# Optimization experiments

Measured on AMD Instinct MI355X. Metric: run time of the kernel, lower is better.

Reference implementation:

```python
import jax, jax.numpy as jnp
from jax import lax
import numpy as np

B, S, D, H = 64, 256, 1024, 1024
NEG = -1e9


def setup_inputs() -> dict:
    key = jax.random.key(0)
    ks = jax.random.split(key, 8)
    sd = 1.0 / np.sqrt(D)
    sh = 1.0 / np.sqrt(H + 1)
    return {
        "lstm_features": jax.random.normal(ks[0], (B, S, D), jnp.float32),
        "mask": jnp.ones((B, S), jnp.int32),
        "Wl": jax.random.normal(ks[1], (D, H), jnp.float32) * sd,
        "bl": jnp.zeros((H,), jnp.float32),
        "Wr": jax.random.normal(ks[2], (D, H), jnp.float32) * sd,
        "br": jnp.zeros((H,), jnp.float32),
        "Wbil": jax.random.normal(ks[3], (H + 1, H + 1), jnp.float32) * sh,
        "bbil": jnp.zeros((), jnp.float32),
    }


def _span_scores(lstm_features, Wl, bl, Wr, br, Wbil, bbil):
    # left/right MLPs: Linear + LeakyReLU(0.1) (dropout=0 at inference)
    lefts = jax.nn.leaky_relu(lstm_features @ Wl + bl, 0.1)   # [B,S,H]
    rights = jax.nn.leaky_relu(lstm_features @ Wr + br, 0.1)  # [B,S,H]
    ones = jnp.ones(lefts.shape[:-1] + (1,), lefts.dtype)
    l1 = jnp.concatenate([lefts, ones], axis=-1)   # [B,S,H+1] (use_input_biases=True)
    r1 = jnp.concatenate([rights, ones], axis=-1)
    # bilinear: l1 @ W @ r1^T + bias  -> [B,S,S]
    return jnp.einsum('bsh,hg,btg->bst', l1, Wbil, r1) + bbil


def _cky(scores):
    """CKY over one [S,S] score matrix. chart[i,j]=scores[i,j]+max_s chart[i,s]+chart[s+1,j];
    singleton spans score 0. Returns (chart, best-split table)."""
    n = scores.shape[0]
    idx = jnp.arange(n)
    m = jnp.arange(n - 1)  # split offsets
    chart0 = jnp.zeros((n, n), scores.dtype)
    split0 = jnp.zeros((n, n), jnp.int32)

    def step(carry, w):
        chart, split = carry
        j = idx + w
        jc = jnp.clip(j, 0, n - 1)
        li = jnp.clip(idx[:, None] + m[None, :], 0, n - 1)       # left end
        ri = jnp.clip(idx[:, None] + m[None, :] + 1, 0, n - 1)   # right start
        cand = chart[idx[:, None], li] + chart[ri, jc[:, None]]  # [n, n-1]
        valid = (m[None, :] < w) & (j[:, None] < n)
        cand = jnp.where(valid, cand, NEG)
        val = scores[idx, jc] + jnp.max(cand, axis=1)
        bsplit = (idx + jnp.argmax(cand, axis=1)).astype(jnp.int32)
        ok = j < n
        chart = chart.at[idx, jc].set(jnp.where(ok, val, chart[idx, jc]))
        split = split.at[idx, jc].set(jnp.where(ok, bsplit, split[idx, jc]))
        return (chart, split), None

    (chart, split), _ = lax.scan(step, (chart0, split0), jnp.arange(1, n))
    return chart, split


def _backtrack(split):
    """Extract the n-1 internal spans of the best tree (fixed-size stack, jit-safe)."""
    n = split.shape[0]
    stack = jnp.full((2 * n, 2), -1, jnp.int32).at[0].set(jnp.array([0, n - 1], jnp.int32))
    out = jnp.zeros((n, 2), jnp.int32)

    def body(t, state):
        def do_pop(st):
            stack, top, out, cnt = st
            ij = stack[top - 1]
            i, j = ij[0], ij[1]
            top = top - 1
            out = out.at[cnt].set(ij)
            cnt = cnt + 1
            s = split[i, j]
            stack = stack.at[top].set(jnp.stack([i, s]))          # left child
            top = top + (s > i).astype(jnp.int32)
            stack = stack.at[top].set(jnp.stack([s + 1, j]))      # right child
            top = top + (j > s + 1).astype(jnp.int32)
            return (stack, top, out, cnt)
        return lax.cond(state[1] > 0, do_pop, lambda s: s, state)

    state = (stack, jnp.int32(1), out, jnp.int32(0))
    _, _, out, _ = lax.fori_loop(0, n - 1, body, state)
    return out  # [n,2] (lefts, rights), zero-padded like torch.zeros in original


def reference(lstm_features, mask, Wl, bl, Wr, br, Wbil, bbil):
    scores = _span_scores(lstm_features, Wl, bl, Wr, br, Wbil, bbil)  # [B,S,S]
    _, split = jax.vmap(_cky)(scores)
    spans = jax.vmap(_backtrack)(split)  # [B,S,2]
    ret_lefts = spans[..., 0].astype(jnp.int64)
    ret_rights = spans[..., 1].astype(jnp.int64)
    return ret_lefts, ret_rights
```

## Files before the change

kernel.cpp:

```cpp
#include <hip/hip_runtime.h>
#include <cstdint>


#define Bb 64
#define Ss 256
#define Dd 1024
#define Hh 1024

typedef __attribute__((ext_vector_type(8))) _Float16 f16x8;
typedef __attribute__((ext_vector_type(4))) float f32x4;

__device__ __forceinline__ void split2(float x, unsigned short& h,
                                       unsigned short& l) {
  _Float16 hh = (_Float16)x;
  _Float16 ll = (_Float16)(x - (float)hh);
  h = __builtin_bit_cast(unsigned short, hh);
  l = __builtin_bit_cast(unsigned short, ll);
}

__device__ __forceinline__ void gl_lds16(const void* g, void* l) {
  __builtin_amdgcn_global_load_lds(
      (const __attribute__((address_space(1))) void*)g,
      (__attribute__((address_space(3))) void*)l, 16, 0, 0);
}

__global__ __launch_bounds__(256) void splitw_kernel(
    const float* __restrict__ W, int ldw, unsigned short* __restrict__ O,
    long long plane) {
  int idx = blockIdx.x * 256 + threadIdx.x;
  int n = idx >> 10, k = idx & 1023;
  float x = W[(long long)k * ldw + n];
  unsigned short h, l;
  split2(x, h, l);
  O[idx] = h;
  O[plane + idx] = l;
}

__global__ __launch_bounds__(256) void bilvec_kernel(
    const float* __restrict__ Wbil, float* __restrict__ brow,
    float* __restrict__ bcol, float* __restrict__ corner) {
  int i = blockIdx.x * 256 + threadIdx.x;
  brow[i] = Wbil[1024 * 1025 + i];
  bcol[i] = Wbil[i * 1025 + 1024];
  if (i == 0) corner[0] = Wbil[1024 * 1025 + 1024];
}

__device__ __forceinline__ void pack8(char* dst, const unsigned short* v) {
  uint4 u;
  u.x = (unsigned)v[0] | ((unsigned)v[1] << 16);
  u.y = (unsigned)v[2] | ((unsigned)v[3] << 16);
  u.z = (unsigned)v[4] | ((unsigned)v[5] << 16);
  u.w = (unsigned)v[6] | ((unsigned)v[7] << 16);
  *(uint4*)dst = u;
}

__device__ __forceinline__ void split_store16f(const float* xs, char* lds,
                                               int base, int wa0, int wa1) {
  unsigned short hs[16], ls[16];
#pragma unroll
  for (int i = 0; i < 16; ++i) split2(xs[i], hs[i], ls[i]);
  pack8(&lds[base + wa0], hs);
  pack8(&lds[base + wa1], hs + 8);
  pack8(&lds[base + 8192 + wa0], ls);
  pack8(&lds[base + 8192 + wa1], ls + 8);
}

#define MFMA4(afv, bh, blv, accs, nf)                                        \
  {                                                                          \
    _Pragma("unroll") for (int mf = 0; mf < 4; ++mf) accs[mf][nf] =          \
        __builtin_amdgcn_mfma_f32_16x16x32_f16(afv[0][mf], bh,               \
                                               accs[mf][nf], 0, 0, 0);       \
    _Pragma("unroll") for (int mf = 0; mf < 4; ++mf) accs[mf][nf] =          \
        __builtin_amdgcn_mfma_f32_16x16x32_f16(afv[0][mf], blv,              \
                                               accs[mf][nf], 0, 0, 0);       \
    _Pragma("unroll") for (int mf = 0; mf < 4; ++mf) accs[mf][nf] =          \
        __builtin_amdgcn_mfma_f32_16x16x32_f16(afv[1][mf], bh,               \
                                               accs[mf][nf], 0, 0, 0);       \
    _Pragma("unroll") for (int mf = 0; mf < 4; ++mf) accs[mf][nf] =          \
        __builtin_amdgcn_mfma_f32_16x16x32_f16(afv[1][mf], blv,              \
                                               accs[mf][nf], 0, 0, 0);       \
  }

template <bool LEAKY>
__global__ __launch_bounds__(256, 3) void gemm_mfma_kernel(
    const float* __restrict__ A, const unsigned short* __restrict__ Bsp,
    long long bplane, float* __restrict__ C0, float* __restrict__ C1,
    const float* __restrict__ bias0, const float* __restrict__ bias1) {
  const int m0 = blockIdx.y * 128;
  const int n0 = blockIdx.x * 128;
  __shared__ __align__(16) char lds[49152];
  const int t = threadIdx.x;
  const int L = t & 63, w = t >> 6, q = L >> 4, l15 = L & 15;

  const int ar = t >> 1, ah = t & 1;
  const float* aptr = A + (long long)(m0 + ar) * 1024 + ah * 16;
  const int phiA = ((ar >> 1) ^ (ar >> 3)) & 3;
  const int wa0 = ar * 64 + (((2 * ah + 0) ^ phiA) << 4);
  const int wa1 = ar * 64 + (((2 * ah + 1) ^ phiA) << 4);

  int offA0[4], offB0[4];
#pragma unroll
  for (int f = 0; f < 4; ++f) {
    int rowa = ((w & 1) << 6) + (f << 4) + l15;
    offA0[f] = rowa * 64 + ((q ^ (((rowa >> 1) ^ (rowa >> 3)) & 3)) << 4);
    int rowb = ((w >> 1) << 6) + (f << 4) + l15;
    offB0[f] = rowb * 64 + ((q ^ (((rowb >> 1) ^ (rowb >> 3)) & 3)) << 4);
  }

  const int lrow = L >> 2, lchk = L & 3;
  const unsigned short* bsrc[4];
  int bldso[4];
#pragma unroll
  for (int i = 0; i < 4; ++i) {
    int O = ((w << 2) + i) << 10;
    int s2 = O >> 13;
    int r = ((O & 8191) >> 6) + lrow;
    int phi = ((r >> 1) ^ (r >> 3)) & 3;
    bsrc[i] = Bsp + (long long)s2 * bplane + (long long)(n0 + r) * 1024 +
              ((lchk ^ phi) << 3);
    bldso[i] = O;
  }

  f32x4 acc[4][4];
#pragma unroll
  for (int i = 0; i < 4; ++i)
#pragma unroll
    for (int j = 0; j < 4; ++j) acc[i][j] = (f32x4){0.f, 0.f, 0.f, 0.f};

#pragma unroll
  for (int i = 0; i < 4; ++i) gl_lds16(bsrc[i], &lds[16384 + bldso[i]]);
  float4 a0 = *(const float4*)(aptr + 0);
  float4 a1 = *(const float4*)(aptr + 4);
  float4 a2 = *(const float4*)(aptr + 8);
  float4 a3 = *(const float4*)(aptr + 12);

  int cur = 0;
  for (int k0 = 0; k0 < 1024; k0 += 32) {
    {
      float xs[16] = {a0.x, a0.y, a0.z, a0.w, a1.x, a1.y, a1.z, a1.w,
                      a2.x, a2.y, a2.z, a2.w, a3.x, a3.y, a3.z, a3.w};
      split_store16f(xs, lds, 0, wa0, wa1);
    }
    asm volatile("s_waitcnt vmcnt(0) lgkmcnt(0)\n\ts_barrier" ::: "memory");
    if (k0 < 992) {
      a0 = *(const float4*)(aptr + k0 + 32);
      a1 = *(const float4*)(aptr + k0 + 36);
      a2 = *(const float4*)(aptr + k0 + 40);
      a3 = *(const float4*)(aptr + k0 + 44);
      const int bn = 16384 + ((cur ^ 1) << 14);
#pragma unroll
      for (int i = 0; i < 4; ++i)
        gl_lds16(bsrc[i] + k0 + 32, &lds[bn + bldso[i]]);
    }
    const int bb = 16384 + (cur << 14);
    f16x8 af[2][4];
#pragma unroll
    for (int s = 0; s < 2; ++s)
#pragma unroll
      for (int f = 0; f < 4; ++f)
        af[s][f] = *(const f16x8*)&lds[s * 8192 + offA0[f]];
#pragma unroll
    for (int nf = 0; nf < 4; ++nf) {
      f16x8 bh = *(const f16x8*)&lds[bb + offB0[nf]];
      f16x8 bl = *(const f16x8*)&lds[bb + 8192 + offB0[nf]];
      MFMA4(af, bh, bl, acc, nf);
    }
    asm volatile("s_waitcnt lgkmcnt(0)\n\ts_barrier" ::: "memory");
    cur ^= 1;
  }

  const bool isR = (n0 >= 1024);
  float* Co = isR ? C1 : C0;
  const float* bp = isR ? bias1 : bias0;
  const int nc0 = n0 & 1023;
#pragma unroll
  for (int nf = 0; nf < 4; ++nf) {
    int col = nc0 + ((w >> 1) << 6) + (nf << 4) + l15;
    float bz = bp[col];
#pragma unroll
    for (int mf = 0; mf < 4; ++mf) {
#pragma unroll
      for (int r = 0; r < 4; ++r) {
        int row = m0 + ((w & 1) << 6) + (mf << 4) + (q << 2) + r;
        float x = acc[mf][nf][r] + bz;
        if (LEAKY) x = (x > 0.f) ? x : 0.1f * x;
        Co[(long long)row * 1024 + col] = x;
      }
    }
  }
}

__global__ __launch_bounds__(256, 3) void gemmnt_mfma_kernel(
    const float* __restrict__ A, const float* __restrict__ B,
    float* __restrict__ C, const float* __restrict__ rowAdd,
    const float* __restrict__ scal) {
  const int bz = blockIdx.z;
  A += (long long)bz * 256 * 1024;
  B += (long long)bz * 256 * 1024;
  C += (long long)bz * 256 * 256;
  const int m0 = blockIdx.y * 128;
  const int n0 = blockIdx.x * 128;
  __shared__ __align__(16) char lds[32768];
  const int t = threadIdx.x;
  const int L = t & 63, w = t >> 6, q = L >> 4, l15 = L & 15;

  const int ar = t >> 1, ah = t & 1;
  const float* aptr = A + (long long)(m0 + ar) * 1024 + ah * 16;
  const float* bptr = B + (long long)(n0 + ar) * 1024 + ah * 16;
  const int phiA = ((ar >> 1) ^ (ar >> 3)) & 3;
  const int wa0 = ar * 64 + (((2 * ah + 0) ^ phiA) << 4);
  const int wa1 = ar * 64 + (((2 * ah + 1) ^ phiA) << 4);

  int offA0[4], offB0[4];
#pragma unroll
  for (int f = 0; f < 4; ++f) {
    int rowa = ((w & 1) << 6) + (f << 4) + l15;
    offA0[f] = rowa * 64 + ((q ^ (((rowa >> 1) ^ (rowa >> 3)) & 3)) << 4);
    int rowb = ((w >> 1) << 6) + (f << 4) + l15;
    offB0[f] =
        16384 + rowb * 64 + ((q ^ (((rowb >> 1) ^ (rowb >> 3)) & 3)) << 4);
  }

  f32x4 acc[4][4];
#pragma unroll
  for (int i = 0; i < 4; ++i)
#pragma unroll
    for (int j = 0; j < 4; ++j) acc[i][j] = (f32x4){0.f, 0.f, 0.f, 0.f};

  float4 a0 = *(const float4*)(aptr + 0);
  float4 a1 = *(const float4*)(aptr + 4);
  float4 a2 = *(const float4*)(aptr + 8);
  float4 a3 = *(const float4*)(aptr + 12);
  float4 b0 = *(const float4*)(bptr + 0);
  float4 b1 = *(const float4*)(bptr + 4);
  float4 b2 = *(const float4*)(bptr + 8);
  float4 b3 = *(const float4*)(bptr + 12);

  for (int k0 = 0; k0 < 1024; k0 += 32) {
    {
      float xs[16] = {a0.x, a0.y, a0.z, a0.w, a1.x, a1.y, a1.z, a1.w,
                      a2.x, a2.y, a2.z, a2.w, a3.x, a3.y, a3.z, a3.w};
      split_store16f(xs, lds, 0, wa0, wa1);
      float ys[16] = {b0.x, b0.y, b0.z, b0.w, b1.x, b1.y, b1.z, b1.w,
                      b2.x, b2.y, b2.z, b2.w, b3.x, b3.y, b3.z, b3.w};
      split_store16f(ys, lds, 16384, wa0, wa1);
    }
    asm volatile("s_waitcnt lgkmcnt(0)\n\ts_barrier" ::: "memory");
    if (k0 < 992) {
      a0 = *(const float4*)(aptr + k0 + 32);
      a1 = *(const float4*)(aptr + k0 + 36);
      a2 = *(const float4*)(aptr + k0 + 40);
      a3 = *(const float4*)(aptr + k0 + 44);
      b0 = *(const float4*)(bptr + k0 + 32);
      b1 = *(const float4*)(bptr + k0 + 36);
      b2 = *(const float4*)(bptr + k0 + 40);
      b3 = *(const float4*)(bptr + k0 + 44);
    }
    f16x8 af[2][4];
#pragma unroll
    for (int s = 0; s < 2; ++s)
#pragma unroll
      for (int f = 0; f < 4; ++f)
        af[s][f] = *(const f16x8*)&lds[s * 8192 + offA0[f]];
#pragma unroll
    for (int nf = 0; nf < 4; ++nf) {
      f16x8 bh = *(const f16x8*)&lds[offB0[nf]];
      f16x8 bl = *(const f16x8*)&lds[8192 + offB0[nf]];
      MFMA4(af, bh, bl, acc, nf);
    }
    asm volatile("s_waitcnt lgkmcnt(0)\n\ts_barrier" ::: "memory");
  }

  const float sc_add = scal[0];
#pragma unroll
  for (int mf = 0; mf < 4; ++mf) {
#pragma unroll
    for (int r = 0; r < 4; ++r) {
      int row = m0 + ((w & 1) << 6) + (mf << 4) + (q << 2) + r;
      float radd = sc_add + rowAdd[(long long)bz * 256 + row];
#pragma unroll
      for (int nf = 0; nf < 4; ++nf) {
        int col = n0 + ((w >> 1) << 6) + (nf << 4) + l15;
        C[(long long)row * 256 + col] = acc[mf][nf][r] + radd;
      }
    }
  }
}

__global__ __launch_bounds__(64) void colvec_kernel(
    const float* __restrict__ lefts, const float* __restrict__ bcol,
    const float* __restrict__ corner, float* __restrict__ tmpb) {
  int row = blockIdx.x;
  int lane = threadIdx.x;
  const float* a = lefts + (long long)row * Hh;
  float s = 0.f;
#pragma unroll
  for (int h = lane; h < Hh; h += 64) s = fmaf(a[h], bcol[h], s);
#pragma unroll
  for (int off = 32; off > 0; off >>= 1) s += __shfl_down(s, off, 64);
  if (lane == 0) tmpb[row] = s + corner[0];
}

__global__ __launch_bounds__(1024) void cky_kernel(
    const float* __restrict__ scores,
    uint8_t* __restrict__ Sws,
    int* __restrict__ out)
{
  const int b = blockIdx.x;
  const int t = threadIdx.x;
  const int n = Ss;
  const float* sc = scores + (long long)b * n * n;
  uint8_t* SP = Sws + (long long)b * 32896;

  __shared__ float Dch[32896];
  __shared__ float pv[2][2048];
  __shared__ uint8_t pmv[2][2048];
  __shared__ int stk[256];

  const int offT[10] = {0,    256,  511,  765,  1018,
                        1270, 1521, 1771, 2020, 2268};

  if (t < n) {
    out[b * n + t] = 0;
    out[Bb * n + b * n + t] = 0;
    Dch[t] = 0.f;
  }

  float PS[10];
  PS[0] = 0.f;
#pragma unroll
  for (int w = 1; w <= 9; ++w) {
    int ic = t;
    if (ic > 255 - w) ic = 255 - w;
    PS[w] = sc[ic * 257 + w];
  }
  asm volatile("s_waitcnt lgkmcnt(0)\n\ts_barrier" ::: "memory");

#pragma unroll
  for (int w = 1; w <= 9; ++w) {
    const int nv = n - w;
    if (t < nv) {
      float bb = Dch[offT[w - 1] + t + 1];
      int bm = 0;
#pragma unroll
      for (int m = 1; m < 9; ++m) {
        if (m >= w) break;
        float c = Dch[offT[m] + t] + Dch[offT[w - 1 - m] + t + m + 1];
        if (c > bb) { bb = c; bm = m; }
      }
      const int off = w * 256 - ((w * (w - 1)) >> 1);
      Dch[off + t] = PS[w] + bb;
      SP[off + t] = (uint8_t)bm;
    }
    asm volatile("s_waitcnt lgkmcnt(0)\n\ts_barrier" ::: "memory");
  }

  auto run_b = [&](int W0b, int pbuf) {
    const int cnv = n - W0b - 4;
    int jb, gb, u, delta, lgGHL, SLOTG;
    if (cnv > 128) {
      const int p = t >> 7;
      jb = 3 - (p >> 1);
      gb = 1 - (p & 1);
      u = t & 127;
      delta = 128;
      lgGHL = 1;
      SLOTG = 256;
    } else {
      const int wid = t >> 6;
      jb = 3 - (wid >> 2);
      gb = 3 - (wid & 3);
      u = t & 63;
      delta = (cnv > 64) ? 64 : 0;
      lgGHL = 2;
      SLOTG = 128;
    }
    const int Wb = W0b + 4 + jb;
    const int nvb = n - Wb;
    int cnt = W0b - jb - 4;
    if (cnt < 0) cnt = 0;
    const int per = (cnt + (1 << lgGHL) - 1) >> lgGHL;
    const int mlo = jb + 4;
    int ml = mlo + gb * per;
    int mh = mlo + cnt;
    {
      int e = ml + per;
      if (e < mh) mh = e;
    }
    float b0 = -3.0e38f, b1 = -3.0e38f;
    int m0i = ml, m1i = ml;
    if (u < nvb && ml < mh) {
      int al = ml * n - ((ml * (ml - 1)) >> 1) + u;
      const int kr = Wb - 1 - ml;
      int ar = kr * n - ((kr * (kr - 1)) >> 1) + u + ml + 1;
      int dl = n - ml;
      int dr = n - Wb + ml + 1;
      if (delta) {
#pragma unroll 2
        for (int m = ml; m < mh; ++m) {
          float l0 = Dch[al], l1 = Dch[al + delta];
          float r0 = Dch[ar], r1 = Dch[ar + delta];
          float c0 = l0 + r0, c1 = l1 + r1;
          if (c0 > b0) { b0 = c0; m0i = m; }
          if (c1 > b1) { b1 = c1; m1i = m; }
          al += dl;
          ar -= dr;
          --dl;
          ++dr;
        }
      } else {
#pragma unroll 4
        for (int m = ml; m < mh; ++m) {
          float c = Dch[al] + Dch[ar];
          if (c > b0) { b0 = c; m0i = m; }
          al += dl;
          ar -= dr;
          --dl;
          ++dr;
        }
      }
    }
    const int slot = jb * 512 + gb * SLOTG + u;
    pv[pbuf][slot] = b0;
    pmv[pbuf][slot] = (uint8_t)m0i;
    if (delta) {
      pv[pbuf][slot + delta] = b1;
      pmv[pbuf][slot + delta] = (uint8_t)m1i;
    }
  };

  run_b(6, 0);
  asm volatile("s_waitcnt lgkmcnt(0)\n\ts_barrier" ::: "memory");

  const int wv = t >> 6, lane = t & 63;
  const int tcell = 61 * wv + lane;

  float scA[4];
#pragma unroll
  for (int j = 0; j < 4; ++j) {
    const int Wn = 10 + j;
    int ic = tcell;
    if (ic > 255 - Wn) ic = 255 - Wn;
    if (ic < 0) ic = 0;
    scA[j] = sc[ic * 257 + Wn];
  }

  for (int s = 3; s <= 64; ++s) {
    const int W0 = 4 * s - 2;
    const int nv1 = n - W0;
    const int pb = s & 1, po = pb ^ 1;
    const int nb = (nv1 + 60) / 61;

    float P4[4] = {0.f, 0.f, 0.f, 0.f};
    if (s < 64 && wv < nb) {
#pragma unroll
      for (int j = 0; j < 4; ++j) {
        const int Wn = W0 + 4 + j;
        int ic = tcell;
        if (ic > 255 - Wn) ic = 255 - Wn;
        if (ic < 0) ic = 0;
        P4[j] = sc[ic * 257 + Wn];
      }
    }

    if (wv < nb) {
      const int tc = (tcell < nv1) ? tcell : (nv1 - 1);
      const float* pvo = pv[po];
      const uint8_t* pmo = pmv[po];
      int GHa, SGa;
      if (nv1 > 128) { GHa = 2; SGa = 256; } else { GHa = 4; SGa = 128; }
      int offPB[4], offCB[4];
#pragma unroll
      for (int d = 0; d < 4; ++d) {
        const int dg = W0 - 4 + d;
        offPB[d] = dg * 256 - ((dg * (dg - 1)) >> 1);
        const int cg = W0 + d;
        offCB[d] = cg * 256 - ((cg * (cg - 1)) >> 1);
      }
      float VAL0, VAL1, VAL2, VAL3;
      float SH01, SH02, SH03, SH11, SH12, SH21;
      {
        const int W = W0;
        float bb = Dch[offPB[3] + tc + 1];
        int bm = 0;
#pragma unroll
        for (int dm = 1; dm < 4; ++dm) {
          const int m = dm;
          float c = Dch[offT[m] + tc] + Dch[offPB[3 - dm] + tc + m + 1];
          if (c > bb) { bb = c; bm = m; }
        }
#pragma unroll
        for (int g = 0; g < 4; ++g) {
          if (g >= GHa) break;
          const int sl = g * SGa + tc;
          float x = pvo[sl];
          if (x > bb) { bb = x; bm = pmo[sl]; }
        }
#pragma unroll
        for (int dr = 3; dr >= 0; --dr) {
          const int r = dr;
          const int m = W - 1 - r;
          float right = (r == 0) ? 0.f : Dch[offT[r] + tc + W - r];
          float c = Dch[offPB[3 - dr] + tc] + right;
          if (c > bb) { bb = c; bm = m; }
        }
        VAL0 = scA[0] + bb;
        if (tcell < nv1) {
          Dch[offCB[0] + tcell] = VAL0;
          SP[offCB[0] + tcell] = (uint8_t)bm;
        }
        SH01 = __shfl_down(VAL0, 1, 64);
        SH02 = __shfl_down(VAL0, 2, 64);
        SH03 = __shfl_down(VAL0, 3, 64);
      }
      {
        const int W = W0 + 1;
        float bb = SH01;
        int bm = 0;
#pragma unroll
        for (int dm = 0; dm < 4; ++dm) {
          const int m = 1 + dm;
          float c = Dch[offT[m] + tc] + Dch[offPB[3 - dm] + tc + m + 1];
          if (c > bb) { bb = c; bm = m; }
        }
#pragma unroll
        for (int g = 0; g < 4; ++g) {
          if (g >= GHa) break;
          const int sl = 512 + g * SGa + tc;
          float x = pvo[sl];
          if (x > bb) { bb = x; bm = pmo[sl]; }
        }
#pragma unroll
        for (int dr = 3; dr >= 0; --dr) {
          const int r = 1 + dr;
          const int m = W - 1 - r;
          float c = Dch[offPB[3 - dr] + tc] + Dch[offT[r] + tc + W - r];
          if (c > bb) { bb = c; bm = m; }
        }
        if (VAL0 > bb) { bb = VAL0; bm = W - 1; }
        VAL1 = scA[1] + bb;
        if (lane <= 62 && tcell < nv1 - 1) {
          Dch[offCB[1] + tcell] = VAL1;
          SP[offCB[1] + tcell] = (uint8_t)bm;
        }
        SH11 = __shfl_down(VAL1, 1, 64);
        SH12 = __shfl_down(VAL1, 2, 64);
      }
      {
        const int W = W0 + 2;
        float bb = SH11;
        int bm = 0;
        {
          float c = Dch[offT[1] + tc] + SH02;
          if (c > bb) { bb = c; bm = 1; }
        }
#pragma unroll
        for (int dm = 0; dm < 4; ++dm) {
          const int m = 2 + dm;
          float c = Dch[offT[m] + tc] + Dch[offPB[3 - dm] + tc + m + 1];
          if (c > bb) { bb = c; bm = m; }
        }
#pragma unroll
        for (int g = 0; g < 4; ++g) {
          if (g >= GHa) break;
          const int sl = 1024 + g * SGa + tc;
          float x = pvo[sl];
          if (x > bb) { bb = x; bm = pmo[sl]; }
        }
#pragma unroll
        for (int dr = 3; dr >= 0; --dr) {
          const int r = 2 + dr;
          const int m = W - 1 - r;
          float c = Dch[offPB[3 - dr] + tc] + Dch[offT[r] + tc + W - r];
          if (c > bb) { bb = c; bm = m; }
        }
        {
          float c = VAL0 + Dch[offT[1] + tc + W - 1];
          if (c > bb) { bb = c; bm = W - 2; }
        }
        if (VAL1 > bb) { bb = VAL1; bm = W - 1; }
        VAL2 = scA[2] + bb;
        if (lane <= 61 && tcell < nv1 - 2) {
          Dch[offCB[2] + tcell] = VAL2;
          SP[offCB[2] + tcell] = (uint8_t)bm;
        }
        SH21 = __shfl_down(VAL2, 1, 64);
      }
      {
        const int W = W0 + 3;
        float bb = SH21;
        int bm = 0;
        {
          float c = Dch[offT[1] + tc] + SH12;
          if (c > bb) { bb = c; bm = 1; }
        }
        {
          float c = Dch[offT[2] + tc] + SH03;
          if (c > bb) { bb = c; bm = 2; }
        }
#pragma unroll
        for (int dm = 0; dm < 4; ++dm) {
          const int m = 3 + dm;
          float c = Dch[offT[m] + tc] + Dch[offPB[3 - dm] + tc + m + 1];
          if (c > bb) { bb = c; bm = m; }
        }
#pragma unroll
        for (int g = 0; g < 4; ++g) {
          if (g >= GHa) break;
          const int sl = 1536 + g * SGa + tc;
          float x = pvo[sl];
          if (x > bb) { bb = x; bm = pmo[sl]; }
        }
#pragma unroll
        for (int dr = 3; dr >= 0; --dr) {
          const int r = 3 + dr;
          const int m = W - 1 - r;
          float c = Dch[offPB[3 - dr] + tc] + Dch[offT[r] + tc + W - r];
          if (c > bb) { bb = c; bm = m; }
        }
        {
          float c = VAL0 + Dch[offT[2] + tc + W - 2];
          if (c > bb) { bb = c; bm = W - 3; }
        }
        {
          float c = VAL1 + Dch[offT[1] + tc + W - 1];
          if (c > bb) { bb = c; bm = W - 2; }
        }
        if (VAL2 > bb) { bb = VAL2; bm = W - 1; }
        VAL3 = scA[3] + bb;
        if (lane <= 60 && tcell < nv1 - 3) {
          Dch[offCB[3] + tcell] = VAL3;
          SP[offCB[3] + tcell] = (uint8_t)bm;
        }
      }
    }

    if (s < 64) run_b(W0, pb);

    asm volatile("s_waitcnt lgkmcnt(0)\n\ts_barrier" ::: "memory");
#pragma unroll
    for (int j = 0; j < 4; ++j) scA[j] = P4[j];
  }

  asm volatile("s_waitcnt vmcnt(0) lgkmcnt(0)\n\ts_barrier" ::: "memory");
  uint8_t* spl = (uint8_t*)Dch;
  for (int idx = t; idx < 32896; idx += 1024) spl[idx] = SP[idx];
  asm volatile("s_waitcnt vmcnt(0) lgkmcnt(0)\n\ts_barrier" ::: "memory");
  if (t == 0) {
    int top = 0;
    stk[top++] = (0 << 16) | (n - 1);
    int cnt = 0;
    for (int step = 0; step < n - 1; ++step) {
      if (top > 0) {
        int ij = stk[--top];
        int ii = ij >> 16, jj = ij & 0xffff;
        out[b * n + cnt] = ii;
        out[Bb * n + b * n + cnt] = jj;
        ++cnt;
        int k = jj - ii;
        int s2 = ii + (int)spl[k * n - ((k * (k - 1)) >> 1) + ii];
        stk[top] = (ii << 16) | s2;
        if (s2 > ii) ++top;
        stk[top] = ((s2 + 1) << 16) | jj;
        if (jj > s2 + 1) ++top;
      }
    }
  }
}

extern "C" void kernel_launch(void* const* d_in, const int* in_sizes, int n_in,
                              void* d_out, int out_size, void* d_ws,
                              size_t ws_size, hipStream_t stream) {
  const float* X = (const float*)d_in[0];
  const float* Wl = (const float*)d_in[2];
  const float* bl = (const float*)d_in[3];
  const float* Wr = (const float*)d_in[4];
  const float* br = (const float*)d_in[5];
  const float* Wbil = (const float*)d_in[6];
  const float* bbil = (const float*)d_in[7];
  int* out = (int*)d_out;

  float* ws = (float*)d_ws;
  float* lefts = ws;
  float* rights = lefts + 16777216;
  float* tmpA = rights + 16777216;
  float* scoresP = tmpA + 16777216;
  float* tmpb = scoresP + 4194304;
  float* browp = tmpb + 16384;
  float* bcolp = browp + 1024;
  float* cornerp = bcolp + 1024;
  unsigned short* Wlrt = (unsigned short*)(cornerp + 4);
  unsigned short* Wct = Wlrt + 2LL * 2097152;
  uint8_t* SPp = (uint8_t*)(Wct + 2LL * 1048576);

  splitw_kernel<<<dim3(4096), 256, 0, stream>>>(Wl, 1024, Wlrt, 2097152);
  splitw_kernel<<<dim3(4096), 256, 0, stream>>>(Wr, 1024, Wlrt + 1048576,
                                                2097152);
  splitw_kernel<<<dim3(4096), 256, 0, stream>>>(Wbil, 1025, Wct, 1048576);
  bilvec_kernel<<<dim3(4), 256, 0, stream>>>(Wbil, browp, bcolp, cornerp);

  dim3 gLR(16, 128);
  gemm_mfma_kernel<true><<<gLR, 256, 0, stream>>>(X, Wlrt, 2097152LL, lefts,
                                                  rights, bl, br);

  colvec_kernel<<<dim3(16384), 64, 0, stream>>>(lefts, bcolp, cornerp, tmpb);

  dim3 gA(8, 128);
  gemm_mfma_kernel<false><<<gA, 256, 0, stream>>>(lefts, Wct, 1048576LL, tmpA,
                                                  tmpA, browp, browp);

  dim3 g3(2, 2, 64);
  gemmnt_mfma_kernel<<<g3, 256, 0, stream>>>(tmpA, rights, scoresP, tmpb,
                                             bbil);

  cky_kernel<<<dim3(Bb), dim3(1024), 0, stream>>>(scoresP, SPp, out);
}
```

Before: 865.2 us.

## Pre-split X into fp16 hi/lo planes and stream both operands via LDS DMA

Adds a pass that splits the fp32 input features into fp16 high and low planes once, stored in the scratch buffer that later holds tmpA. The left/right projection GEMM is replaced by a new kernel that loads both A and B split planes straight into LDS with global_load_lds and double buffering. This removes the per-tile fp32-to-fp16 split in registers, at the cost of an extra pass that reads X and writes 2x fp16 planes. LDS use rises to 64KB, which limits occupancy to two blocks per CU.

```diff
diff --git a/kernel.cpp b/kernel.cpp
--- a/kernel.cpp
+++ b/kernel.cpp
@@ -34,6 +34,25 @@
   split2(x, h, l);
   O[idx] = h;
   O[plane + idx] = l;
+}
+
+__global__ __launch_bounds__(256) void splitx_kernel(
+    const float* __restrict__ X, unsigned short* __restrict__ O,
+    long long plane) {
+  long long i4 = ((long long)blockIdx.x * 256 + threadIdx.x) * 4;
+  float4 v = *(const float4*)(X + i4);
+  unsigned short h[4], l[4];
+  split2(v.x, h[0], l[0]);
+  split2(v.y, h[1], l[1]);
+  split2(v.z, h[2], l[2]);
+  split2(v.w, h[3], l[3]);
+  uint2 hp, lp;
+  hp.x = (unsigned)h[0] | ((unsigned)h[1] << 16);
+  hp.y = (unsigned)h[2] | ((unsigned)h[3] << 16);
+  lp.x = (unsigned)l[0] | ((unsigned)l[1] << 16);
+  lp.y = (unsigned)l[2] | ((unsigned)l[3] << 16);
+  *(uint2*)(O + i4) = hp;
+  *(uint2*)(O + plane + i4) = lp;
 }
 
 __global__ __launch_bounds__(256) void bilvec_kernel(
@@ -80,6 +99,106 @@
         __builtin_amdgcn_mfma_f32_16x16x32_f16(afv[1][mf], blv,              \
                                                accs[mf][nf], 0, 0, 0);       \
   }
+
+template <bool LEAKY>
+__global__ __launch_bounds__(256, 2) void gemm_sp_kernel(
+    const unsigned short* __restrict__ Asp, long long aplane,
+    const unsigned short* __restrict__ Bsp, long long bplane,
+    float* __restrict__ C0, float* __restrict__ C1,
+    const float* __restrict__ bias0, const float* __restrict__ bias1) {
+  const int m0 = blockIdx.y * 128;
+  const int n0 = blockIdx.x * 128;
+  __shared__ __align__(16) char lds[65536];
+  const int t = threadIdx.x;
+  const int L = t & 63, w = t >> 6, q = L >> 4, l15 = L & 15;
+
+  int offA0[4], offB0[4];
+#pragma unroll
+  for (int f = 0; f < 4; ++f) {
+    int rowa = ((w & 1) << 6) + (f << 4) + l15;
+    offA0[f] = rowa * 64 + ((q ^ (((rowa >> 1) ^ (rowa >> 3)) & 3)) << 4);
+    int rowb = ((w >> 1) << 6) + (f << 4) + l15;
+    offB0[f] = rowb * 64 + ((q ^ (((rowb >> 1) ^ (rowb >> 3)) & 3)) << 4);
+  }
+
+  const int lrow = L >> 2, lchk = L & 3;
+  const unsigned short* asrc[4];
+  const unsigned short* bsrc[4];
+  int ldso[4];
+#pragma unroll
+  for (int i = 0; i < 4; ++i) {
+    int O = ((w << 2) + i) << 10;
+    int s2 = O >> 13;
+    int r = ((O & 8191) >> 6) + lrow;
+    int phi = ((r >> 1) ^ (r >> 3)) & 3;
+    asrc[i] = Asp + (long long)s2 * aplane + (long long)(m0 + r) * 1024 +
+              ((lchk ^ phi) << 3);
+    bsrc[i] = Bsp + (long long)s2 * bplane + (long long)(n0 + r) * 1024 +
+              ((lchk ^ phi) << 3);
+    ldso[i] = O;
+  }
+
+  f32x4 acc[4][4];
+#pragma unroll
+  for (int i = 0; i < 4; ++i)
+#pragma unroll
+    for (int j = 0; j < 4; ++j) acc[i][j] = (f32x4){0.f, 0.f, 0.f, 0.f};
+
+#pragma unroll
+  for (int i = 0; i < 4; ++i) gl_lds16(asrc[i], &lds[ldso[i]]);
+#pragma unroll
+  for (int i = 0; i < 4; ++i) gl_lds16(bsrc[i], &lds[32768 + ldso[i]]);
+  asm volatile("s_waitcnt vmcnt(0)\n\ts_barrier" ::: "memory");
+
+  int cur = 0;
+  for (int k0 = 0; k0 < 1024; k0 += 32) {
+    if (k0 < 992) {
+      const int an = (cur ^ 1) << 14;
+#pragma unroll
+      for (int i = 0; i < 4; ++i)
+        gl_lds16(asrc[i] + k0 + 32, &lds[an + ldso[i]]);
+#pragma unroll
+      for (int i = 0; i < 4; ++i)
+        gl_lds16(bsrc[i] + k0 + 32, &lds[32768 + an + ldso[i]]);
+    }
+    const int ab = cur << 14;
+    const int bbase = 32768 + ab;
+    f16x8 af[2][4];
+#pragma unroll
+    for (int s = 0; s < 2; ++s)
+#pragma unroll
+      for (int f = 0; f < 4; ++f)
+        af[s][f] = *(const f16x8*)&lds[ab + s * 8192 + offA0[f]];
+#pragma unroll
+    for (int nf = 0; nf < 4; ++nf) {
+      f16x8 bh = *(const f16x8*)&lds[bbase + offB0[nf]];
+      f16x8 bl = *(const f16x8*)&lds[bbase + 8192 + offB0[nf]];
+      MFMA4(af, bh, bl, acc, nf);
+    }
+    asm volatile("s_waitcnt vmcnt(0) lgkmcnt(0)\n\ts_barrier" ::: "memory");
+    cur ^= 1;
+  }
+
+  const bool isR = (n0 >= 1024);
+  float* Co = isR ? C1 : C0;
+  const float* bp = isR ? bias1 : bias0;
+  const int nc0 = n0 & 1023;
+#pragma unroll
+  for (int nf = 0; nf < 4; ++nf) {
+    int col = nc0 + ((w >> 1) << 6) + (nf << 4) + l15;
+    float bz = bp[col];
+#pragma unroll
+    for (int mf = 0; mf < 4; ++mf) {
+#pragma unroll
+      for (int r = 0; r < 4; ++r) {
+        int row = m0 + ((w & 1) << 6) + (mf << 4) + (q << 2) + r;
+        float x = acc[mf][nf][r] + bz;
+        if (LEAKY) x = (x > 0.f) ? x : 0.1f * x;
+        Co[(long long)row * 1024 + col] = x;
+      }
+    }
+  }
+}
 
 template <bool LEAKY>
 __global__ __launch_bounds__(256, 3) void gemm_mfma_kernel(
@@ -693,15 +812,18 @@
   unsigned short* Wct = Wlrt + 2LL * 2097152;
   uint8_t* SPp = (uint8_t*)(Wct + 2LL * 1048576);
 
+  unsigned short* Xsp = (unsigned short*)tmpA;
+
   splitw_kernel<<<dim3(4096), 256, 0, stream>>>(Wl, 1024, Wlrt, 2097152);
   splitw_kernel<<<dim3(4096), 256, 0, stream>>>(Wr, 1024, Wlrt + 1048576,
                                                 2097152);
   splitw_kernel<<<dim3(4096), 256, 0, stream>>>(Wbil, 1025, Wct, 1048576);
   bilvec_kernel<<<dim3(4), 256, 0, stream>>>(Wbil, browp, bcolp, cornerp);
+  splitx_kernel<<<dim3(16384), 256, 0, stream>>>(X, Xsp, 16777216LL);
 
   dim3 gLR(16, 128);
-  gemm_mfma_kernel<true><<<gLR, 256, 0, stream>>>(X, Wlrt, 2097152LL, lefts,
-                                                  rights, bl, br);
+  gemm_sp_kernel<true><<<gLR, 256, 0, stream>>>(
+      Xsp, 16777216LL, Wlrt, 2097152LL, lefts, rights, bl, br);
 
   colvec_kernel<<<dim3(16384), 64, 0, stream>>>(lefts, bcolp, cornerp, tmpb);
 
```

Result: no change. 876.5 us (+1.3%).

## Widen CKY diagonal blocking from 4 to 8 widths per barrier step

Applied to the files above, without the earlier changes.

Restructures the CKY wavefront so each block step processes 8 span widths instead of 4, with a 15-width direct prologue and a generic unrolled inner loop that uses wave shuffles for intra-block dependencies. This halves the number of block-level barriers and pipelined stages (about 30 instead of about 62). The cost is more redundant work and shuffles per step, lower lane utilisation (57 useful cells per wave instead of 61), and a rebalanced run_b partition whose long-range split search is less parallel.

```diff
diff --git a/kernel.cpp b/kernel.cpp
--- a/kernel.cpp
+++ b/kernel.cpp
@@ -317,19 +317,21 @@
   __shared__ uint8_t pmv[2][2048];
   __shared__ int stk[256];
 
-  const int offT[10] = {0,    256,  511,  765,  1018,
-                        1270, 1521, 1771, 2020, 2268};
+  const int offT[16] = {0,    256,  511,  765,  1018, 1270, 1521, 1771,
+                        2020, 2268, 2515, 2761, 3006, 3250, 3493, 3735};
 
   if (t < n) {
     out[b * n + t] = 0;
     out[Bb * n + b * n + t] = 0;
     Dch[t] = 0.f;
   }
-
-  float PS[10];
+  pv[1][t] = -3.0e38f;
+  pv[1][t + 1024] = -3.0e38f;
+
+  float PS[16];
   PS[0] = 0.f;
 #pragma unroll
-  for (int w = 1; w <= 9; ++w) {
+  for (int w = 1; w <= 15; ++w) {
     int ic = t;
     if (ic > 255 - w) ic = 255 - w;
     PS[w] = sc[ic * 257 + w];
@@ -337,53 +339,50 @@
   asm volatile("s_waitcnt lgkmcnt(0)\n\ts_barrier" ::: "memory");
 
 #pragma unroll
-  for (int w = 1; w <= 9; ++w) {
-    const int nv = n - w;
-    if (t < nv) {
+  for (int w = 1; w <= 15; ++w) {
+    if (t < 256 - w) {
       float bb = Dch[offT[w - 1] + t + 1];
       int bm = 0;
 #pragma unroll
-      for (int m = 1; m < 9; ++m) {
+      for (int m = 1; m < 15; ++m) {
         if (m >= w) break;
         float c = Dch[offT[m] + t] + Dch[offT[w - 1 - m] + t + m + 1];
         if (c > bb) { bb = c; bm = m; }
       }
-      const int off = w * 256 - ((w * (w - 1)) >> 1);
-      Dch[off + t] = PS[w] + bb;
-      SP[off + t] = (uint8_t)bm;
+      Dch[offT[w] + t] = PS[w] + bb;
+      SP[offT[w] + t] = (uint8_t)bm;
     }
     asm volatile("s_waitcnt lgkmcnt(0)\n\ts_barrier" ::: "memory");
   }
 
   auto run_b = [&](int W0b, int pbuf) {
-    const int cnv = n - W0b - 4;
-    int jb, gb, u, delta, lgGHL, SLOTG;
+    const int cnv = n - W0b - 8;
+    int jb, gb, u, delta;
     if (cnv > 128) {
-      const int p = t >> 7;
-      jb = 3 - (p >> 1);
-      gb = 1 - (p & 1);
+      jb = 7 - (t >> 7);
+      gb = 0;
       u = t & 127;
       delta = 128;
-      lgGHL = 1;
-      SLOTG = 256;
     } else {
       const int wid = t >> 6;
-      jb = 3 - (wid >> 2);
-      gb = 3 - (wid & 3);
+      jb = 7 - (wid >> 1);
+      gb = wid & 1;
       u = t & 63;
       delta = (cnv > 64) ? 64 : 0;
-      lgGHL = 2;
-      SLOTG = 128;
-    }
-    const int Wb = W0b + 4 + jb;
+    }
+    const int Wb = W0b + 8 + jb;
     const int nvb = n - Wb;
-    int cnt = W0b - jb - 4;
+    int cnt = W0b - jb - 8;
     if (cnt < 0) cnt = 0;
-    const int per = (cnt + (1 << lgGHL) - 1) >> lgGHL;
-    const int mlo = jb + 4;
-    int ml = mlo + gb * per;
-    int mh = mlo + cnt;
-    {
+    const int mlo = jb + 8;
+    int ml, mh;
+    if (cnv > 128) {
+      ml = mlo;
+      mh = mlo + cnt;
+    } else {
+      const int per = (cnt + 1) >> 1;
+      ml = mlo + gb * per;
+      mh = mlo + cnt;
       int e = ml + per;
       if (e < mh) mh = e;
     }
@@ -396,7 +395,7 @@
       int dl = n - ml;
       int dr = n - Wb + ml + 1;
       if (delta) {
-#pragma unroll 2
+#pragma unroll 4
         for (int m = ml; m < mh; ++m) {
           float l0 = Dch[al], l1 = Dch[al + delta];
           float r0 = Dch[ar], r1 = Dch[ar + delta];
@@ -409,7 +408,7 @@
           ++dr;
         }
       } else {
-#pragma unroll 4
+#pragma unroll 8
         for (int m = ml; m < mh; ++m) {
           float c = Dch[al] + Dch[ar];
           if (c > b0) { b0 = c; m0i = m; }
@@ -420,7 +419,7 @@
         }
       }
     }
-    const int slot = jb * 512 + gb * SLOTG + u;
+    const int slot = jb * 256 + gb * 128 + u;
     pv[pbuf][slot] = b0;
     pmv[pbuf][slot] = (uint8_t)m0i;
     if (delta) {
@@ -429,37 +428,33 @@
     }
   };
 
-  run_b(6, 0);
-  asm volatile("s_waitcnt lgkmcnt(0)\n\ts_barrier" ::: "memory");
-
   const int wv = t >> 6, lane = t & 63;
-  const int tcell = 61 * wv + lane;
-
-  float scA[4];
-#pragma unroll
-  for (int j = 0; j < 4; ++j) {
-    const int Wn = 10 + j;
+  const int tcell = 57 * wv + lane;
+
+  float scA[8];
+#pragma unroll
+  for (int j = 0; j < 8; ++j) {
+    const int Wn = 16 + j;
     int ic = tcell;
     if (ic > 255 - Wn) ic = 255 - Wn;
-    if (ic < 0) ic = 0;
     scA[j] = sc[ic * 257 + Wn];
   }
 
-  for (int s = 3; s <= 64; ++s) {
-    const int W0 = 4 * s - 2;
+  for (int s = 2; s <= 31; ++s) {
+    const int W0 = 8 * s;
     const int nv1 = n - W0;
     const int pb = s & 1, po = pb ^ 1;
-    const int nb = (nv1 + 60) / 61;
-
-    float P4[4] = {0.f, 0.f, 0.f, 0.f};
-    if (s < 64 && wv < nb) {
-#pragma unroll
-      for (int j = 0; j < 4; ++j) {
-        const int Wn = W0 + 4 + j;
+    const int nb = (nv1 + 56) / 57;
+
+    float P8[8] = {0.f, 0.f, 0.f, 0.f, 0.f, 0.f, 0.f, 0.f};
+    if (s < 31 && wv < nb) {
+#pragma unroll
+      for (int j = 0; j < 8; ++j) {
+        const int Wn = W0 + 8 + j;
         int ic = tcell;
         if (ic > 255 - Wn) ic = 255 - Wn;
         if (ic < 0) ic = 0;
-        P4[j] = sc[ic * 257 + Wn];
+        P8[j] = sc[ic * 257 + Wn];
       }
     }
 
@@ -467,179 +462,80 @@
       const int tc = (tcell < nv1) ? tcell : (nv1 - 1);
       const float* pvo = pv[po];
       const uint8_t* pmo = pmv[po];
-      int GHa, SGa;
-      if (nv1 > 128) { GHa = 2; SGa = 256; } else { GHa = 4; SGa = 128; }
-      int offPB[4], offCB[4];
-#pragma unroll
-      for (int d = 0; d < 4; ++d) {
-        const int dg = W0 - 4 + d;
+      const bool RA = (nv1 > 128);
+      int offPB[8], offCB[8];
+#pragma unroll
+      for (int d = 0; d < 8; ++d) {
+        const int dg = W0 - 8 + d;
         offPB[d] = dg * 256 - ((dg * (dg - 1)) >> 1);
         const int cg = W0 + d;
         offCB[d] = cg * 256 - ((cg * (cg - 1)) >> 1);
       }
-      float VAL0, VAL1, VAL2, VAL3;
-      float SH01, SH02, SH03, SH11, SH12, SH21;
-      {
-        const int W = W0;
-        float bb = Dch[offPB[3] + tc + 1];
+      float VAL[8];
+#pragma unroll
+      for (int j = 0; j < 8; ++j) {
+        const int W = W0 + j;
+        float bb;
         int bm = 0;
-#pragma unroll
-        for (int dm = 1; dm < 4; ++dm) {
-          const int m = dm;
-          float c = Dch[offT[m] + tc] + Dch[offPB[3 - dm] + tc + m + 1];
+        if (j == 0) {
+          bb = Dch[offPB[7] + tc + 1];
+        } else {
+          bb = __shfl_down(VAL[j - 1], 1, 64);
+        }
+#pragma unroll
+        for (int m = 1; m < 8; ++m) {
+          if (m >= j) break;
+          float c = Dch[offT[m] + tc] + __shfl_down(VAL[j - 1 - m], m + 1, 64);
           if (c > bb) { bb = c; bm = m; }
         }
 #pragma unroll
-        for (int g = 0; g < 4; ++g) {
-          if (g >= GHa) break;
-          const int sl = g * SGa + tc;
+        for (int m2 = 0; m2 < 8; ++m2) {
+          const int m = j + m2;
+          if (m == 0) continue;
+          float c = Dch[offT[m] + tc] + Dch[offPB[7 - m2] + tc + m + 1];
+          if (c > bb) { bb = c; bm = m; }
+        }
+        if (RA) {
+          const int sl = j * 256 + tc;
           float x = pvo[sl];
           if (x > bb) { bb = x; bm = pmo[sl]; }
-        }
-#pragma unroll
-        for (int dr = 3; dr >= 0; --dr) {
-          const int r = dr;
-          const int m = W - 1 - r;
-          float right = (r == 0) ? 0.f : Dch[offT[r] + tc + W - r];
-          float c = Dch[offPB[3 - dr] + tc] + right;
+        } else {
+#pragma unroll
+          for (int g = 0; g < 2; ++g) {
+            const int sl = j * 256 + g * 128 + tc;
+            float x = pvo[sl];
+            if (x > bb) { bb = x; bm = pmo[sl]; }
+          }
+        }
+#pragma unroll
+        for (int d = 0; d < 8; ++d) {
+          const int m = W0 - 8 + d;
+          const int rp = j + 7 - d;
+          float right = (rp == 0) ? 0.f : Dch[offT[rp] + tc + W - rp];
+          float c = Dch[offPB[d] + tc] + right;
           if (c > bb) { bb = c; bm = m; }
         }
-        VAL0 = scA[0] + bb;
-        if (tcell < nv1) {
-          Dch[offCB[0] + tcell] = VAL0;
-          SP[offCB[0] + tcell] = (uint8_t)bm;
-        }
-        SH01 = __shfl_down(VAL0, 1, 64);
-        SH02 = __shfl_down(VAL0, 2, 64);
-        SH03 = __shfl_down(VAL0, 3, 64);
-      }
-      {
-        const int W = W0 + 1;
-        float bb = SH01;
-        int bm = 0;
-#pragma unroll
-        for (int dm = 0; dm < 4; ++dm) {
-          const int m = 1 + dm;
-          float c = Dch[offT[m] + tc] + Dch[offPB[3 - dm] + tc + m + 1];
-          if (c > bb) { bb = c; bm = m; }
-        }
-#pragma unroll
-        for (int g = 0; g < 4; ++g) {
-          if (g >= GHa) break;
-          const int sl = 512 + g * SGa + tc;
-          float x = pvo[sl];
-          if (x > bb) { bb = x; bm = pmo[sl]; }
-        }
-#pragma unroll
-        for (int dr = 3; dr >= 0; --dr) {
-          const int r = 1 + dr;
-          const int m = W - 1 - r;
-          float c = Dch[offPB[3 - dr] + tc] + Dch[offT[r] + tc + W - r];
-          if (c > bb) { bb = c; bm = m; }
-        }
-        if (VAL0 > bb) { bb = VAL0; bm = W - 1; }
-        VAL1 = scA[1] + bb;
-        if (lane <= 62 && tcell < nv1 - 1) {
-          Dch[offCB[1] + tcell] = VAL1;
-          SP[offCB[1] + tcell] = (uint8_t)bm;
-        }
-        SH11 = __shfl_down(VAL1, 1, 64);
-        SH12 = __shfl_down(VAL1, 2, 64);
-      }
-      {
-        const int W = W0 + 2;
-        float bb = SH11;
-        int bm = 0;
-        {
-          float c = Dch[offT[1] + tc] + SH02;
-          if (c > bb) { bb = c; bm = 1; }
-        }
-#pragma unroll
-        for (int dm = 0; dm < 4; ++dm) {
-          const int m = 2 + dm;
-          float c = Dch[offT[m] + tc] + Dch[offPB[3 - dm] + tc + m + 1];
-          if (c > bb) { bb = c; bm = m; }
-        }
-#pragma unroll
-        for (int g = 0; g < 4; ++g) {
-          if (g >= GHa) break;
-          const int sl = 1024 + g * SGa + tc;
-          float x = pvo[sl];
-          if (x > bb) { bb = x; bm = pmo[sl]; }
-        }
-#pragma unroll
-        for (int dr = 3; dr >= 0; --dr) {
-          const int r = 2 + dr;
-          const int m = W - 1 - r;
-          float c = Dch[offPB[3 - dr] + tc] + Dch[offT[r] + tc + W - r];
-          if (c > bb) { bb = c; bm = m; }
-        }
-        {
-          float c = VAL0 + Dch[offT[1] + tc + W - 1];
-          if (c > bb) { bb = c; bm = W - 2; }
-        }
-        if (VAL1 > bb) { bb = VAL1; bm = W - 1; }
-        VAL2 = scA[2] + bb;
-        if (lane <= 61 && tcell < nv1 - 2) {
-          Dch[offCB[2] + tcell] = VAL2;
-          SP[offCB[2] + tcell] = (uint8_t)bm;
-        }
-        SH21 = __shfl_down(VAL2, 1, 64);
-      }
-      {
-        const int W = W0 + 3;
-        float bb = SH21;
-        int bm = 0;
-        {
-          float c = Dch[offT[1] + tc] + SH12;
-          if (c > bb) { bb = c; bm = 1; }
-        }
-        {
-          float c = Dch[offT[2] + tc] + SH03;
-          if (c > bb) { bb = c; bm = 2; }
-        }
-#pragma unroll
-        for (int dm = 0; dm < 4; ++dm) {
-          const int m = 3 + dm;
-          float c = Dch[offT[m] + tc] + Dch[offPB[3 - dm] + tc + m + 1];
-          if (c > bb) { bb = c; bm = m; }
-        }
-#pragma unroll
-        for (int g = 0; g < 4; ++g) {
-          if (g >= GHa) break;
-          const int sl = 1536 + g * SGa + tc;
-          float x = pvo[sl];
-          if (x > bb) { bb = x; bm = pmo[sl]; }
-        }
-#pragma unroll
-        for (int dr = 3; dr >= 0; --dr) {
-          const int r = 3 + dr;
-          const int m = W - 1 - r;
-          float c = Dch[offPB[3 - dr] + tc] + Dch[offT[r] + tc + W - r];
-          if (c > bb) { bb = c; bm = m; }
-        }
-        {
-          float c = VAL0 + Dch[offT[2] + tc + W - 2];
-          if (c > bb) { bb = c; bm = W - 3; }
-        }
-        {
-          float c = VAL1 + Dch[offT[1] + tc + W - 1];
-          if (c > bb) { bb = c; bm = W - 2; }
-        }
-        if (VAL2 > bb) { bb = VAL2; bm = W - 1; }
-        VAL3 = scA[3] + bb;
-        if (lane <= 60 && tcell < nv1 - 3) {
-          Dch[offCB[3] + tcell] = VAL3;
-          SP[offCB[3] + tcell] = (uint8_t)bm;
-        }
-      }
-    }
-
-    if (s < 64) run_b(W0, pb);
+#pragma unroll
+        for (int e = 0; e < 8; ++e) {
+          if (e >= j) break;
+          const int rp = j - 1 - e;
+          float right = (rp == 0) ? 0.f : Dch[offT[rp] + tc + W - rp];
+          float c = VAL[e] + right;
+          if (c > bb) { bb = c; bm = W0 + e; }
+        }
+        VAL[j] = scA[j] + bb;
+        if (lane <= 63 - j && tcell < nv1 - j) {
+          Dch[offCB[j] + tcell] = VAL[j];
+          SP[offCB[j] + tcell] = (uint8_t)bm;
+        }
+      }
+    }
+
+    if (s < 31) run_b(W0, pb);
 
     asm volatile("s_waitcnt lgkmcnt(0)\n\ts_barrier" ::: "memory");
 #pragma unroll
-    for (int j = 0; j < 4; ++j) scA[j] = P4[j];
+    for (int j = 0; j < 8; ++j) scA[j] = P8[j];
   }
 
   asm volatile("s_waitcnt vmcnt(0) lgkmcnt(0)\n\ts_barrier" ::: "memory");
```

Result: no change. 863.4 us (-0.2%).
